# Optimization experiments

Hardware: AMD Instinct MI355X
Metric: run time of the kernel (lower is better)

The kernel has to match this reference:

```python
import jax, jax.numpy as jnp
import numpy as np

NUM_EXPERTS = 8
AUX_LOSS_COEF = 0.01


def setup_inputs() -> dict:
    key = jax.random.key(0)
    ks = jax.random.split(key, 5)
    B, S, D, E, H = 4, 2048, 1024, NUM_EXPERTS, 4096
    scale = 0.02  # typical init scale so gelu/softmax stay in sane ranges
    return {
        "hidden_states": jax.random.normal(ks[0], (B, S, D), dtype=jnp.float32),
        "router_w": jax.random.normal(ks[1], (D, E), dtype=jnp.float32) * scale,
        "router_b": jnp.zeros((E,), dtype=jnp.float32),
        "w1": jax.random.normal(ks[2], (E, D, H), dtype=jnp.float32) * scale,
        "b1": jnp.zeros((E, H), dtype=jnp.float32),
        "w2": jax.random.normal(ks[3], (E, H, D), dtype=jnp.float32) * scale,
        "b2": jnp.zeros((E, D), dtype=jnp.float32),
    }


def reference(hidden_states, router_w, router_b, w1, b1, w2, b2):
    B, S, D = hidden_states.shape
    E = w1.shape[0]
    x = hidden_states.reshape(-1, D)  # [T, D] flattened tokens

    # Switch router: top-1 expert, combine weight = softmax prob of chosen expert
    logits = x @ router_w + router_b                      # [T, E]
    probs = jax.nn.softmax(logits, axis=-1)               # [T, E]
    sel = jnp.argmax(logits, axis=-1)                     # [T] int
    gate = jnp.take_along_axis(probs, sel[:, None], axis=1)[:, 0]  # [T]

    # Expert FFNs: per-expert Linear -> gelu -> Linear, masked top-1 combine.
    # Loop is over the small fixed expert count (structurally distinct weights).
    out = jnp.zeros_like(x)
    for e in range(E):
        h = jax.nn.gelu(x @ w1[e] + b1[e])                # [T, H]
        ye = h @ w2[e] + b2[e]                            # [T, D]
        mask = (sel == e).astype(x.dtype)
        out = out + (mask * gate)[:, None] * ye

    # Switch load-balancing auxiliary loss
    mean_probs = probs.mean(axis=0)                       # [E]
    assignments = jnp.mean(jax.nn.one_hot(sel, E, dtype=x.dtype), axis=0)  # [E]
    aux_loss = jnp.sum(mean_probs * assignments) * E
    total_loss = AUX_LOSS_COEF * aux_loss

    return out.reshape(B, S, D), total_loss
```

## Files before the change

kernel.cpp:

```cpp
#include <hip/hip_runtime.h>
#include <cstdint>

typedef __bf16 bf16_t;
typedef __attribute__((ext_vector_type(8))) __bf16 bf16x8;
typedef __attribute__((ext_vector_type(4))) float f32x4;
typedef unsigned short ushort_t;

#define TOKENS 8192
#define DIM 1024
#define HID 4096
#define NEXP 8


__device__ __forceinline__ void gl_lds16(const void* g, void* l) {
  __builtin_amdgcn_global_load_lds(
      (__attribute__((address_space(1))) void*)(void*)g,
      (__attribute__((address_space(3))) void*)l, 16, 0, 0);
}

__device__ __forceinline__ float gelu_fast(float x) {
  float x2 = x * x;
  float z2 = x * (1.59576912f + 0.07135482f * x2);
  float e = __expf(-z2);
  return x * __builtin_amdgcn_rcpf(1.f + e);
}

template <int N>
__device__ __forceinline__ void pwait() {
  __builtin_amdgcn_sched_barrier(0);
  if constexpr (N == 4) asm volatile("s_waitcnt vmcnt(4)" ::: "memory");
  else if constexpr (N == 3) asm volatile("s_waitcnt vmcnt(3)" ::: "memory");
  else asm volatile("s_waitcnt vmcnt(0)" ::: "memory");
  __builtin_amdgcn_sched_barrier(0);
  __builtin_amdgcn_s_barrier();
  __builtin_amdgcn_sched_barrier(0);
}

__device__ __forceinline__ int xcd_chunk(int f, int nwg) {
  int q = nwg >> 3, r = nwg & 7;
  int xcd = f & 7, pos = f >> 3;
  return (xcd < r) ? (xcd * (q + 1) + pos) : (r * (q + 1) + (xcd - r) * q + pos);
}

__global__ void router_kernel(const float* __restrict__ x, const float* __restrict__ rw,
                              const float* __restrict__ rbias, bf16_t* __restrict__ xb,
                              int* __restrict__ sel, float* __restrict__ gate,
                              float* __restrict__ pprob, int* __restrict__ pcnt) {
  __shared__ float sprob[NEXP];
  __shared__ int scnt[NEXP];
  int t = threadIdx.x, lane = t & 63, wave = t >> 6;
  if (t < NEXP) { sprob[t] = 0.f; scnt[t] = 0; }
  __syncthreads();
  int tok = blockIdx.x * 4 + wave;
  const float* xp = x + (size_t)tok * DIM + lane * 16;
  float acc[NEXP];
#pragma unroll
  for (int e = 0; e < NEXP; ++e) acc[e] = 0.f;
  ushort_t xv[16];
#pragma unroll
  for (int j = 0; j < 16; j += 4) {
    float4 v = *(const float4*)(xp + j);
    const float* wr = rw + (size_t)(lane * 16 + j) * NEXP;
    float c[4] = {v.x, v.y, v.z, v.w};
#pragma unroll
    for (int d = 0; d < 4; ++d) {
      xv[j + d] = __builtin_bit_cast(ushort_t, (bf16_t)c[d]);
#pragma unroll
      for (int e = 0; e < NEXP; ++e) acc[e] += c[d] * wr[d * NEXP + e];
    }
  }
  {
    uint4* xop = (uint4*)(xb + (size_t)tok * DIM + lane * 16);
    xop[0] = ((uint4*)xv)[0];
    xop[1] = ((uint4*)xv)[1];
  }
#pragma unroll
  for (int s = 1; s < 64; s <<= 1)
#pragma unroll
    for (int e = 0; e < NEXP; ++e) acc[e] += __shfl_xor(acc[e], s);
  if (lane == 0) {
    float lg[NEXP];
#pragma unroll
    for (int e = 0; e < NEXP; ++e) lg[e] = acc[e] + rbias[e];
    float mx = lg[0]; int am = 0;
#pragma unroll
    for (int e = 1; e < NEXP; ++e) if (lg[e] > mx) { mx = lg[e]; am = e; }
    float p[NEXP]; float se = 0.f;
#pragma unroll
    for (int e = 0; e < NEXP; ++e) { p[e] = __expf(lg[e] - mx); se += p[e]; }
    float inv = 1.f / se;
#pragma unroll
    for (int e = 0; e < NEXP; ++e) { p[e] *= inv; atomicAdd(&sprob[e], p[e]); }
    sel[tok] = am;
    gate[tok] = p[am];
    atomicAdd(&scnt[am], 1);
  }
  __syncthreads();
  if (t < NEXP) {
    pprob[blockIdx.x * NEXP + t] = sprob[t];
    pcnt[blockIdx.x * NEXP + t] = scnt[t];
  }
}

__global__ void tcvt2_kernel(const float* __restrict__ w1, const float* __restrict__ w2,
                             bf16_t* __restrict__ w1t, bf16_t* __restrict__ w2t) {
  __shared__ float tile[64][65];
  int y = blockIdx.y;
  int which = y >> 3, e = y & 7;
  int R = which ? HID : DIM;
  int C = which ? DIM : HID;
  const float* src = (which ? w2 : w1) + (size_t)e * R * C;
  bf16_t* dst = (which ? w2t : w1t) + (size_t)e * R * C;
  int cbt = C >> 6;
  int rt = blockIdx.x / cbt, ct = blockIdx.x % cbt;
  int rb = rt * 64, cb = ct * 64;
  int t = threadIdx.x;
  int r = t >> 2, cq = (t & 3) * 16;
  const float* sp = src + (size_t)(rb + r) * C + cb + cq;
#pragma unroll
  for (int j = 0; j < 16; j += 4) {
    float4 v = *(const float4*)(sp + j);
    tile[r][cq + j + 0] = v.x; tile[r][cq + j + 1] = v.y;
    tile[r][cq + j + 2] = v.z; tile[r][cq + j + 3] = v.w;
  }
  __syncthreads();
  int oc = t >> 2, orr = (t & 3) * 16;
  ushort_t tmp[16];
#pragma unroll
  for (int j = 0; j < 16; ++j) {
    bf16_t b = (bf16_t)tile[orr + j][oc];
    tmp[j] = __builtin_bit_cast(ushort_t, b);
  }
  uint4* dp = (uint4*)(dst + (size_t)(cb + oc) * R + rb + orr);
  dp[0] = ((uint4*)tmp)[0];
  dp[1] = ((uint4*)tmp)[1];
}

__global__ void reduce_kernel(const float* __restrict__ pprob, const int* __restrict__ pcnt,
                              int nb, int* __restrict__ meta, float* __restrict__ loss_out) {
  __shared__ float fred[256];
  __shared__ int ired[256];
  int t = threadIdx.x;
  int e = t & 7, i0 = t >> 3;
  float fs = 0.f; int is = 0;
  for (int i = i0; i < nb; i += 32) { fs += pprob[i * 8 + e]; is += pcnt[i * 8 + e]; }
  fred[t] = fs; ired[t] = is;
  __syncthreads();
  if (t < NEXP) {
    float tp = 0.f; int tc = 0;
    for (int j = 0; j < 32; ++j) { tp += fred[j * 8 + t]; tc += ired[j * 8 + t]; }
    meta[t] = tc;
    fred[t] = tp;
    meta[16 + t] = 0;
  }
  __syncthreads();
  if (t == 0) {
    int off = 0; float loss = 0.f; int s1 = 0, s2 = 0;
    for (int q = 0; q < NEXP; ++q) {
      int c = meta[q];
      meta[8 + q] = off;
      int nt1 = (c + 255) >> 8;
      for (int m = 0; m < nt1; ++m) meta[32 + s1++] = (q << 16) | m;
      int nt2 = (c + 127) >> 7;
      for (int m = 0; m < nt2; ++m) meta[96 + s2++] = (q << 16) | m;
      off += c;
      loss += (fred[q] / (float)TOKENS) * ((float)c / (float)TOKENS);
    }
    meta[24] = s1;
    meta[25] = s2;
    *loss_out = loss * (float)NEXP * 0.01f;
  }
}

__global__ void scatter_kernel(const int* __restrict__ sel, int* __restrict__ meta,
                               int* __restrict__ idxl) {
  int tok = blockIdx.x * 256 + threadIdx.x;
  int lane = threadIdx.x & 63;
  int e = sel[tok];
  const int* offsets = meta + 8;
  int* cursors = meta + 16;
#pragma unroll
  for (int ex = 0; ex < NEXP; ++ex) {
    unsigned long long mask = __ballot(e == ex);
    if (e == ex) {
      int leader = __ffsll(mask) - 1;
      int total = __popcll(mask);
      int rank = __popcll(mask & ((1ull << lane) - 1ull));
      int base = 0;
      if (lane == leader) base = atomicAdd(&cursors[ex], total);
      base = __shfl(base, leader);
      idxl[offsets[ex] + base + rank] = tok;
    }
  }
}

#define STG1(Q, KT) do {                                                     \
    int _kb = (KT) * 32;                                                     \
    gl_lds16(apA0 + _kb, L1 + (Q) * 16384 + (wave * 16) * 32);               \
    gl_lds16(apA1 + _kb, L1 + (Q) * 16384 + (128 + wave * 16) * 32);         \
    gl_lds16(bpB0 + _kb, L1 + (Q) * 16384 + 8192 + (wave * 16) * 32);        \
    gl_lds16(bpB1 + _kb, L1 + (Q) * 16384 + 8192 + (128 + wave * 16) * 32);  \
  } while (0)

#define CMP1(Q) do {                                                         \
    const bf16_t* Ab = L1 + (Q) * 16384;                                     \
    const bf16_t* Bb = Ab + 8192;                                            \
    bf16x8 bv[4];                                                            \
    _Pragma("unroll")                                                        \
    for (int n = 0; n < 4; ++n)                                              \
      bv[n] = *(const bf16x8*)&Bb[(wcol * 64 + n * 16 + l15) * 32 + ks];     \
    __builtin_amdgcn_s_setprio(1);                                           \
    _Pragma("unroll")                                                        \
    for (int m = 0; m < 8; ++m) {                                            \
      bf16x8 af = *(const bf16x8*)&Ab[(wrow * 128 + m * 16 + l15) * 32 + ks];\
      _Pragma("unroll")                                                      \
      for (int n = 0; n < 4; ++n)                                            \
        acc[m][n] = __builtin_amdgcn_mfma_f32_16x16x32_bf16(af, bv[n], acc[m][n], 0, 0, 0); \
    }                                                                        \
    __builtin_amdgcn_s_setprio(0);                                           \
  } while (0)

__global__ __launch_bounds__(512, 2) void gemm1_kernel(
    const bf16_t* __restrict__ xb, const bf16_t* __restrict__ w1t,
    const float* __restrict__ b1, const int* __restrict__ idxl,
    const int* __restrict__ meta, bf16_t* __restrict__ h) {
  int S = gridDim.x;
  int f = blockIdx.y * S + blockIdx.x;
  int lf = xcd_chunk(f, S * gridDim.y);
  int slot = lf % S, nt = lf / S;
  if (slot >= meta[24]) return;
  int tm = meta[32 + slot];
  int e = tm >> 16, mt = tm & 0xffff;
  int cnt = meta[e];
  int off = meta[8 + e];
  int mBase = mt * 256;
  int nBase = nt * 256;
  __shared__ bf16_t L1[49152];
  int t = threadIdx.x, lane = t & 63, wave = t >> 6;
  int l15 = lane & 15, g = lane >> 4;
  int wrow = wave >> 2, wcol = wave & 3;
  int ks = (g ^ (l15 & 3)) * 8;
  f32x4 acc[8][4];
#pragma unroll
  for (int m = 0; m < 8; ++m)
#pragma unroll
    for (int n = 0; n < 4; ++n) acc[m][n] = (f32x4){0.f, 0.f, 0.f, 0.f};

  int lr = lane >> 2;
  int koff = ((lane & 3) ^ (lr & 3)) * 8;
  int c1 = cnt - 1;
  int r0 = wave * 16 + lr;
  int s0 = mBase + r0; s0 = s0 < c1 ? s0 : c1;
  int s1 = mBase + 128 + r0; s1 = s1 < c1 ? s1 : c1;
  const bf16_t* apA0 = xb + (size_t)idxl[off + s0] * DIM + koff;
  const bf16_t* apA1 = xb + (size_t)idxl[off + s1] * DIM + koff;
  const bf16_t* wb = w1t + (size_t)e * HID * DIM;
  const bf16_t* bpB0 = wb + (size_t)(nBase + r0) * DIM + koff;
  const bf16_t* bpB1 = wb + (size_t)(nBase + 128 + r0) * DIM + koff;

  STG1(0, 0);
  STG1(1, 1);
  pwait<4>();
#pragma unroll 1
  for (int kt = 0; kt < 30; kt += 3) {
    STG1(2, kt + 2); CMP1(0); pwait<4>();
    STG1(0, kt + 3); CMP1(1); pwait<4>();
    STG1(1, kt + 4); CMP1(2); pwait<4>();
  }
  CMP1(0);
  pwait<0>();
  CMP1(1);

  float bias[4];
#pragma unroll
  for (int n = 0; n < 4; ++n) bias[n] = b1[e * HID + nBase + wcol * 64 + n * 16 + l15];
#pragma unroll
  for (int m = 0; m < 8; ++m) {
    int rb0 = mBase + wrow * 128 + m * 16 + g * 4;
#pragma unroll
    for (int j = 0; j < 4; ++j) {
      int r = rb0 + j;
      if (r < cnt) {
        bf16_t* hp = h + (size_t)(off + r) * HID + nBase + wcol * 64 + l15;
#pragma unroll
        for (int n = 0; n < 4; ++n)
          hp[n * 16] = (bf16_t)gelu_fast(acc[m][n][j] + bias[n]);
      }
    }
  }
}

#define STG2(Q, KT) do {                                                     \
    int _kb = (KT) * 32;                                                     \
    gl_lds16(apA0 + _kb, L2 + (Q) * 12288 + (wave * 16) * 32);               \
    gl_lds16(bpB0 + _kb, L2 + (Q) * 12288 + 4096 + (wave * 16) * 32);        \
    gl_lds16(bpB1 + _kb, L2 + (Q) * 12288 + 4096 + (128 + wave * 16) * 32);  \
  } while (0)

#define CMP2(Q) do {                                                         \
    const bf16_t* Ab = L2 + (Q) * 12288;                                     \
    const bf16_t* Bb = Ab + 4096;                                            \
    bf16x8 bv[4];                                                            \
    _Pragma("unroll")                                                        \
    for (int n = 0; n < 4; ++n)                                              \
      bv[n] = *(const bf16x8*)&Bb[(wcol * 64 + n * 16 + l15) * 32 + ks];     \
    __builtin_amdgcn_s_setprio(1);                                           \
    _Pragma("unroll")                                                        \
    for (int m = 0; m < 4; ++m) {                                            \
      bf16x8 af = *(const bf16x8*)&Ab[(wrow * 64 + m * 16 + l15) * 32 + ks]; \
      _Pragma("unroll")                                                      \
      for (int n = 0; n < 4; ++n)                                            \
        acc[m][n] = __builtin_amdgcn_mfma_f32_16x16x32_bf16(af, bv[n], acc[m][n], 0, 0, 0); \
    }                                                                        \
    __builtin_amdgcn_s_setprio(0);                                           \
  } while (0)

__global__ __launch_bounds__(512, 4) void gemm2_kernel(
    const bf16_t* __restrict__ h, const bf16_t* __restrict__ w2t,
    const float* __restrict__ b2, const int* __restrict__ idxl,
    const float* __restrict__ gate, const int* __restrict__ meta,
    float* __restrict__ out) {
  int S = gridDim.x;
  int f = blockIdx.y * S + blockIdx.x;
  int lf = xcd_chunk(f, S * gridDim.y);
  int slot = lf % S, nt = lf / S;
  if (slot >= meta[25]) return;
  int tm = meta[96 + slot];
  int e = tm >> 16, mt = tm & 0xffff;
  int cnt = meta[e];
  int off = meta[8 + e];
  int mBase = mt * 128;
  int nBase = nt * 256;
  __shared__ bf16_t L2[36864];
  int t = threadIdx.x, lane = t & 63, wave = t >> 6;
  int l15 = lane & 15, g = lane >> 4;
  int wrow = wave >> 2, wcol = wave & 3;
  int ks = (g ^ (l15 & 3)) * 8;
  f32x4 acc[4][4];
#pragma unroll
  for (int m = 0; m < 4; ++m)
#pragma unroll
    for (int n = 0; n < 4; ++n) acc[m][n] = (f32x4){0.f, 0.f, 0.f, 0.f};

  int lr = lane >> 2;
  int koff = ((lane & 3) ^ (lr & 3)) * 8;
  int c1 = cnt - 1;
  int r0 = wave * 16 + lr;
  int s0 = mBase + r0; s0 = s0 < c1 ? s0 : c1;
  const bf16_t* apA0 = h + (size_t)(off + s0) * HID + koff;
  const bf16_t* wb = w2t + (size_t)e * DIM * HID;
  const bf16_t* bpB0 = wb + (size_t)(nBase + r0) * HID + koff;
  const bf16_t* bpB1 = wb + (size_t)(nBase + 128 + r0) * HID + koff;

  STG2(0, 0);
  STG2(1, 1);
  pwait<3>();
#pragma unroll 1
  for (int kt = 0; kt < 126; kt += 3) {
    STG2(2, kt + 2); CMP2(0); pwait<3>();
    STG2(0, kt + 3); CMP2(1); pwait<3>();
    STG2(1, kt + 4); CMP2(2); pwait<3>();
  }
  CMP2(0);
  pwait<0>();
  CMP2(1);

  float bias[4];
#pragma unroll
  for (int n = 0; n < 4; ++n) bias[n] = b2[e * DIM + nBase + wcol * 64 + n * 16 + l15];
#pragma unroll
  for (int m = 0; m < 4; ++m) {
    int rb0 = mBase + wrow * 64 + m * 16 + g * 4;
#pragma unroll
    for (int j = 0; j < 4; ++j) {
      int r = rb0 + j;
      if (r < cnt) {
        int tok = idxl[off + r];
        float gg = gate[tok];
        float* op = out + (size_t)tok * DIM + nBase + wcol * 64 + l15;
#pragma unroll
        for (int n = 0; n < 4; ++n)
          op[n * 16] = gg * (acc[m][n][j] + bias[n]);
      }
    }
  }
}

extern "C" void kernel_launch(void* const* d_in, const int* in_sizes, int n_in,
                              void* d_out, int out_size, void* d_ws, size_t ws_size,
                              hipStream_t stream) {
  const float* hs = (const float*)d_in[0];
  const float* rw = (const float*)d_in[1];
  const float* rb = (const float*)d_in[2];
  const float* w1 = (const float*)d_in[3];
  const float* b1 = (const float*)d_in[4];
  const float* w2 = (const float*)d_in[5];
  const float* b2 = (const float*)d_in[6];
  float* out = (float*)d_out;
  char* ws = (char*)d_ws;

  bf16_t* xb   = (bf16_t*)(ws + 0);
  bf16_t* w1t  = (bf16_t*)(ws + 16777216);
  bf16_t* w2t  = (bf16_t*)(ws + 83886080);
  bf16_t* hbuf = (bf16_t*)(ws + 150994944);
  int*   sel   = (int*)  (ws + 220200960);
  float* gate  = (float*)(ws + 220233728);
  int*   idxl  = (int*)  (ws + 220266496);
  float* pprob = (float*)(ws + 220299264);
  int*   pcnt  = (int*)  (ws + 220364800);
  int*   meta  = (int*)  (ws + 220430336);

  router_kernel<<<2048, 256, 0, stream>>>(hs, rw, rb, xb, sel, gate, pprob, pcnt);
  tcvt2_kernel<<<dim3(1024, 16), 256, 0, stream>>>(w1, w2, w1t, w2t);
  reduce_kernel<<<1, 256, 0, stream>>>(pprob, pcnt, 2048, meta, out + (out_size - 1));
  scatter_kernel<<<32, 256, 0, stream>>>(sel, meta, idxl);
  gemm1_kernel<<<dim3(40, 16), 512, 0, stream>>>(xb, w1t, b1, idxl, meta, hbuf);
  gemm2_kernel<<<dim3(72, 4), 512, 0, stream>>>(hbuf, w2t, b2, idxl, gate, meta, out);
}
```

Measured before the change: 396.0 us.

## Shrink gemm1 M-tile to 128 and unify LDS layout across both GEMMs

gemm1 now uses 128-row M tiles, with 72 slots and 4 blocks per CU, sharing a single STG/CMP macro pair with gemm2. The LDS layout changes from a row-major XOR-swizzled 32-wide K layout to a fragment-major layout: each 16-row group stores 512 elements indexed by g*128 + l15*8. Global loads now map one lane per row, with each lane group g covering one 8-wide K chunk. The goal is better occupancy and less padding waste for uneven expert counts, and fewer LDS bank conflicts, in exchange for lower per-block data reuse and more blocks reloading B.

Result: slower. 470.8 us (+18.9%).

```diff
diff --git a/kernel.cpp b/kernel.cpp
--- a/kernel.cpp
+++ b/kernel.cpp
@@ -28,8 +28,7 @@
 template <int N>
 __device__ __forceinline__ void pwait() {
   __builtin_amdgcn_sched_barrier(0);
-  if constexpr (N == 4) asm volatile("s_waitcnt vmcnt(4)" ::: "memory");
-  else if constexpr (N == 3) asm volatile("s_waitcnt vmcnt(3)" ::: "memory");
+  if constexpr (N == 3) asm volatile("s_waitcnt vmcnt(3)" ::: "memory");
   else asm volatile("s_waitcnt vmcnt(0)" ::: "memory");
   __builtin_amdgcn_sched_barrier(0);
   __builtin_amdgcn_s_barrier();
@@ -155,18 +154,15 @@
   }
   __syncthreads();
   if (t == 0) {
-    int off = 0; float loss = 0.f; int s1 = 0, s2 = 0;
+    int off = 0; float loss = 0.f; int s2 = 0;
     for (int q = 0; q < NEXP; ++q) {
       int c = meta[q];
       meta[8 + q] = off;
-      int nt1 = (c + 255) >> 8;
-      for (int m = 0; m < nt1; ++m) meta[32 + s1++] = (q << 16) | m;
       int nt2 = (c + 127) >> 7;
       for (int m = 0; m < nt2; ++m) meta[96 + s2++] = (q << 16) | m;
       off += c;
       loss += (fred[q] / (float)TOKENS) * ((float)c / (float)TOKENS);
     }
-    meta[24] = s1;
     meta[25] = s2;
     *loss_out = loss * (float)NEXP * 0.01f;
   }
@@ -194,25 +190,25 @@
   }
 }
 
-#define STG1(Q, KT) do {                                                     \
+
+#define STG(Q, KT) do {                                                      \
     int _kb = (KT) * 32;                                                     \
-    gl_lds16(apA0 + _kb, L1 + (Q) * 16384 + (wave * 16) * 32);               \
-    gl_lds16(apA1 + _kb, L1 + (Q) * 16384 + (128 + wave * 16) * 32);         \
-    gl_lds16(bpB0 + _kb, L1 + (Q) * 16384 + 8192 + (wave * 16) * 32);        \
-    gl_lds16(bpB1 + _kb, L1 + (Q) * 16384 + 8192 + (128 + wave * 16) * 32);  \
+    gl_lds16(apA + _kb, L + (Q) * 12288 + wave * 512);                       \
+    gl_lds16(bpB0 + _kb, L + (Q) * 12288 + 4096 + wave * 512);               \
+    gl_lds16(bpB1 + _kb, L + (Q) * 12288 + 4096 + (wave + 8) * 512);         \
   } while (0)
 
-#define CMP1(Q) do {                                                         \
-    const bf16_t* Ab = L1 + (Q) * 16384;                                     \
-    const bf16_t* Bb = Ab + 8192;                                            \
+#define CMP(Q) do {                                                          \
+    const bf16_t* Ab = L + (Q) * 12288;                                      \
+    const bf16_t* Bb = Ab + 4096;                                            \
     bf16x8 bv[4];                                                            \
     _Pragma("unroll")                                                        \
     for (int n = 0; n < 4; ++n)                                              \
-      bv[n] = *(const bf16x8*)&Bb[(wcol * 64 + n * 16 + l15) * 32 + ks];     \
+      bv[n] = *(const bf16x8*)&Bb[(wcol * 4 + n) * 512 + g * 128 + l15 * 8]; \
     __builtin_amdgcn_s_setprio(1);                                           \
     _Pragma("unroll")                                                        \
-    for (int m = 0; m < 8; ++m) {                                            \
-      bf16x8 af = *(const bf16x8*)&Ab[(wrow * 128 + m * 16 + l15) * 32 + ks];\
+    for (int m = 0; m < 4; ++m) {                                            \
+      bf16x8 af = *(const bf16x8*)&Ab[(wrow * 4 + m) * 512 + g * 128 + l15 * 8]; \
       _Pragma("unroll")                                                      \
       for (int n = 0; n < 4; ++n)                                            \
         acc[m][n] = __builtin_amdgcn_mfma_f32_16x16x32_bf16(af, bv[n], acc[m][n], 0, 0, 0); \
@@ -220,7 +216,7 @@
     __builtin_amdgcn_s_setprio(0);                                           \
   } while (0)
 
-__global__ __launch_bounds__(512, 2) void gemm1_kernel(
+__global__ __launch_bounds__(512, 4) void gemm1_kernel(
     const bf16_t* __restrict__ xb, const bf16_t* __restrict__ w1t,
     const float* __restrict__ b1, const int* __restrict__ idxl,
     const int* __restrict__ meta, bf16_t* __restrict__ h) {
@@ -228,55 +224,50 @@
   int f = blockIdx.y * S + blockIdx.x;
   int lf = xcd_chunk(f, S * gridDim.y);
   int slot = lf % S, nt = lf / S;
-  if (slot >= meta[24]) return;
-  int tm = meta[32 + slot];
+  if (slot >= meta[25]) return;
+  int tm = meta[96 + slot];
   int e = tm >> 16, mt = tm & 0xffff;
   int cnt = meta[e];
   int off = meta[8 + e];
-  int mBase = mt * 256;
+  int mBase = mt * 128;
   int nBase = nt * 256;
-  __shared__ bf16_t L1[49152];
+  __shared__ bf16_t L[36864];
   int t = threadIdx.x, lane = t & 63, wave = t >> 6;
   int l15 = lane & 15, g = lane >> 4;
   int wrow = wave >> 2, wcol = wave & 3;
-  int ks = (g ^ (l15 & 3)) * 8;
-  f32x4 acc[8][4];
-#pragma unroll
-  for (int m = 0; m < 8; ++m)
+  f32x4 acc[4][4];
+#pragma unroll
+  for (int m = 0; m < 4; ++m)
 #pragma unroll
     for (int n = 0; n < 4; ++n) acc[m][n] = (f32x4){0.f, 0.f, 0.f, 0.f};
 
-  int lr = lane >> 2;
-  int koff = ((lane & 3) ^ (lr & 3)) * 8;
   int c1 = cnt - 1;
-  int r0 = wave * 16 + lr;
-  int s0 = mBase + r0; s0 = s0 < c1 ? s0 : c1;
-  int s1 = mBase + 128 + r0; s1 = s1 < c1 ? s1 : c1;
-  const bf16_t* apA0 = xb + (size_t)idxl[off + s0] * DIM + koff;
-  const bf16_t* apA1 = xb + (size_t)idxl[off + s1] * DIM + koff;
+  int koff = g * 8;
+  int sA = mBase + wave * 16 + l15; sA = sA < c1 ? sA : c1;
+  const bf16_t* apA = xb + (size_t)idxl[off + sA] * DIM + koff;
   const bf16_t* wb = w1t + (size_t)e * HID * DIM;
-  const bf16_t* bpB0 = wb + (size_t)(nBase + r0) * DIM + koff;
-  const bf16_t* bpB1 = wb + (size_t)(nBase + 128 + r0) * DIM + koff;
-
-  STG1(0, 0);
-  STG1(1, 1);
-  pwait<4>();
+  const bf16_t* bpB0 = wb + (size_t)(nBase + wave * 16 + l15) * DIM + koff;
+  const bf16_t* bpB1 = wb + (size_t)(nBase + 128 + wave * 16 + l15) * DIM + koff;
+
+  STG(0, 0);
+  STG(1, 1);
+  pwait<3>();
 #pragma unroll 1
   for (int kt = 0; kt < 30; kt += 3) {
-    STG1(2, kt + 2); CMP1(0); pwait<4>();
-    STG1(0, kt + 3); CMP1(1); pwait<4>();
-    STG1(1, kt + 4); CMP1(2); pwait<4>();
-  }
-  CMP1(0);
+    STG(2, kt + 2); CMP(0); pwait<3>();
+    STG(0, kt + 3); CMP(1); pwait<3>();
+    STG(1, kt + 4); CMP(2); pwait<3>();
+  }
+  CMP(0);
   pwait<0>();
-  CMP1(1);
+  CMP(1);
 
   float bias[4];
 #pragma unroll
   for (int n = 0; n < 4; ++n) bias[n] = b1[e * HID + nBase + wcol * 64 + n * 16 + l15];
 #pragma unroll
-  for (int m = 0; m < 8; ++m) {
-    int rb0 = mBase + wrow * 128 + m * 16 + g * 4;
+  for (int m = 0; m < 4; ++m) {
+    int rb0 = mBase + wrow * 64 + m * 16 + g * 4;
 #pragma unroll
     for (int j = 0; j < 4; ++j) {
       int r = rb0 + j;
@@ -289,31 +280,6 @@
     }
   }
 }
-
-#define STG2(Q, KT) do {                                                     \
-    int _kb = (KT) * 32;                                                     \
-    gl_lds16(apA0 + _kb, L2 + (Q) * 12288 + (wave * 16) * 32);               \
-    gl_lds16(bpB0 + _kb, L2 + (Q) * 12288 + 4096 + (wave * 16) * 32);        \
-    gl_lds16(bpB1 + _kb, L2 + (Q) * 12288 + 4096 + (128 + wave * 16) * 32);  \
-  } while (0)
-
-#define CMP2(Q) do {                                                         \
-    const bf16_t* Ab = L2 + (Q) * 12288;                                     \
-    const bf16_t* Bb = Ab + 4096;                                            \
-    bf16x8 bv[4];                                                            \
-    _Pragma("unroll")                                                        \
-    for (int n = 0; n < 4; ++n)                                              \
-      bv[n] = *(const bf16x8*)&Bb[(wcol * 64 + n * 16 + l15) * 32 + ks];     \
-    __builtin_amdgcn_s_setprio(1);                                           \
-    _Pragma("unroll")                                                        \
-    for (int m = 0; m < 4; ++m) {                                            \
-      bf16x8 af = *(const bf16x8*)&Ab[(wrow * 64 + m * 16 + l15) * 32 + ks]; \
-      _Pragma("unroll")                                                      \
-      for (int n = 0; n < 4; ++n)                                            \
-        acc[m][n] = __builtin_amdgcn_mfma_f32_16x16x32_bf16(af, bv[n], acc[m][n], 0, 0, 0); \
-    }                                                                        \
-    __builtin_amdgcn_s_setprio(0);                                           \
-  } while (0)
 
 __global__ __launch_bounds__(512, 4) void gemm2_kernel(
     const bf16_t* __restrict__ h, const bf16_t* __restrict__ w2t,
@@ -331,39 +297,36 @@
   int off = meta[8 + e];
   int mBase = mt * 128;
   int nBase = nt * 256;
-  __shared__ bf16_t L2[36864];
+  __shared__ bf16_t L[36864];
   int t = threadIdx.x, lane = t & 63, wave = t >> 6;
   int l15 = lane & 15, g = lane >> 4;
   int wrow = wave >> 2, wcol = wave & 3;
-  int ks = (g ^ (l15 & 3)) * 8;
   f32x4 acc[4][4];
 #pragma unroll
   for (int m = 0; m < 4; ++m)
 #pragma unroll
     for (int n = 0; n < 4; ++n) acc[m][n] = (f32x4){0.f, 0.f, 0.f, 0.f};
 
-  int lr = lane >> 2;
-  int koff = ((lane & 3) ^ (lr & 3)) * 8;
   int c1 = cnt - 1;
-  int r0 = wave * 16 + lr;
-  int s0 = mBase + r0; s0 = s0 < c1 ? s0 : c1;
-  const bf16_t* apA0 = h + (size_t)(off + s0) * HID + koff;
+  int koff = g * 8;
+  int sA = mBase + wave * 16 + l15; sA = sA < c1 ? sA : c1;
+  const bf16_t* apA = h + (size_t)(off + sA) * HID + koff;
   const bf16_t* wb = w2t + (size_t)e * DIM * HID;
-  const bf16_t* bpB0 = wb + (size_t)(nBase + r0) * HID + koff;
-  const bf16_t* bpB1 = wb + (size_t)(nBase + 128 + r0) * HID + koff;
-
-  STG2(0, 0);
-  STG2(1, 1);
+  const bf16_t* bpB0 = wb + (size_t)(nBase + wave * 16 + l15) * HID + koff;
+  const bf16_t* bpB1 = wb + (size_t)(nBase + 128 + wave * 16 + l15) * HID + koff;
+
+  STG(0, 0);
+  STG(1, 1);
   pwait<3>();
 #pragma unroll 1
   for (int kt = 0; kt < 126; kt += 3) {
-    STG2(2, kt + 2); CMP2(0); pwait<3>();
-    STG2(0, kt + 3); CMP2(1); pwait<3>();
-    STG2(1, kt + 4); CMP2(2); pwait<3>();
-  }
-  CMP2(0);
+    STG(2, kt + 2); CMP(0); pwait<3>();
+    STG(0, kt + 3); CMP(1); pwait<3>();
+    STG(1, kt + 4); CMP(2); pwait<3>();
+  }
+  CMP(0);
   pwait<0>();
-  CMP2(1);
+  CMP(1);
 
   float bias[4];
 #pragma unroll
@@ -414,6 +377,6 @@
   tcvt2_kernel<<<dim3(1024, 16), 256, 0, stream>>>(w1, w2, w1t, w2t);
   reduce_kernel<<<1, 256, 0, stream>>>(pprob, pcnt, 2048, meta, out + (out_size - 1));
   scatter_kernel<<<32, 256, 0, stream>>>(sel, meta, idxl);
-  gemm1_kernel<<<dim3(40, 16), 512, 0, stream>>>(xb, w1t, b1, idxl, meta, hbuf);
+  gemm1_kernel<<<dim3(72, 16), 512, 0, stream>>>(xb, w1t, b1, idxl, meta, hbuf);
   gemm2_kernel<<<dim3(72, 4), 512, 0, stream>>>(hbuf, w2t, b2, idxl, gate, meta, out);
 }
```
